# Kernel tuning notes

Hardware: AMD Instinct MI355X
Metric: run time of the kernel (lower is better)

## Reference

```python
import jax, jax.numpy as jnp
import numpy as np

NUM_BINS = 30
MIN_BW = 0.001
MIN_BH = 0.001
MIN_D = 0.001
LI, UI = 0.0, 1.0   # input bounds
LO, UO = 0.0, 1.0   # output bounds
DERIV_OUT = (UO - LO) / (UI - LI)
EPS = 1e-6


def _cumparams(unnorm, lower, upper, min_size):
    # softmax -> min-size floor -> cumsum -> pad zero -> affine to [lower, upper]
    p = jax.nn.softmax(unnorm, axis=-1)
    p = min_size + (1.0 - min_size * NUM_BINS) * p
    cp = jnp.cumsum(p, axis=-1)
    cp = jnp.pad(cp, [(0, 0), (1, 0)])            # [V, nb+1], starts at 0
    cp = (upper - lower) * cp + lower
    return cp, cp[..., 1:] - cp[..., :-1]         # cum, bin sizes


def _spline_forward(inputs, uw, uh, ud):
    V = uw.shape[0]
    cw, widths = _cumparams(uw, LI, UI, MIN_BW)   # [V, nb+1], [V, nb]
    ch, heights = _cumparams(uh, LO, UO, MIN_BH)

    # boundary derivative constant: softplus(c) = 1 - MIN_D  =>  deriv = 1 at edges
    c = np.log(np.exp(1.0 - MIN_D) - 1.0).astype(np.float32)
    edge = jnp.full((V, 1), c, dtype=uw.dtype)
    derivs = MIN_D + jax.nn.softplus(jnp.concatenate([edge, ud, edge], axis=-1))  # [V, nb+1]

    delta = heights / widths                      # [V, nb]
    cb = cw.at[..., -1].add(EPS)                  # bin-search boundaries

    below = inputs < LI
    above = inputs > UI
    inside = ~(below | above)
    x = jnp.clip(inputs, LI, UI)                  # safe values for masked-out points

    # per-point bin search: [B, V, nb+1] comparison then sum
    bin_idx = jnp.sum(x[..., None] >= cb[None], axis=-1) - 1
    bin_idx = jnp.clip(bin_idx, 0, NUM_BINS - 1)  # [B, V] int

    v = jnp.arange(V)[None, :]
    icw = cw[v, bin_idx]
    ibw = widths[v, bin_idx]
    ich = ch[v, bin_idx]
    idl = delta[v, bin_idx]
    d0 = derivs[v, bin_idx]
    d1 = derivs[v, bin_idx + 1]
    ih = heights[v, bin_idx]

    theta = (x - icw) / ibw
    t1mt = theta * (1.0 - theta)
    den = idl + (d0 + d1 - 2.0 * idl) * t1mt
    out_in = ich + ih * (idl * theta * theta + d0 * t1mt) / den
    numd = (idl * idl) * (d1 * theta * theta + 2.0 * idl * t1mt + d0 * (1.0 - theta) ** 2)
    lad_in = jnp.log(numd) - 2.0 * jnp.log(den)

    out = jnp.where(below, LO + (inputs - LI) * DERIV_OUT,
          jnp.where(above, UO + (inputs - UI) * DERIV_OUT, out_in))
    lad = jnp.where(inside, lad_in, 0.0)
    return out, lad


def setup_inputs() -> dict:
    key = jax.random.key(0)
    k1, k2, k3, k4 = jax.random.split(key, 4)
    B, V = 16384, 512
    inputs = jax.random.uniform(k1, (B, V), dtype=jnp.float32)
    uw = 0.3 * jax.random.normal(k2, (V, NUM_BINS), dtype=jnp.float32)
    uh = 0.3 * jax.random.normal(k3, (V, NUM_BINS), dtype=jnp.float32)
    ud = 0.5405 + 0.1 * jax.random.normal(k4, (V, NUM_BINS - 1), dtype=jnp.float32)
    return {"inputs": inputs, "unnormalized_widths": uw,
            "unnormalized_heights": uh, "unnormalized_derivatives": ud}


def reference(inputs, unnormalized_widths, unnormalized_heights, unnormalized_derivatives):
    return _spline_forward(inputs, unnormalized_widths, unnormalized_heights,
                           unnormalized_derivatives)
```

## Files before the change

### kernel.cpp

```cpp
#include <hip/hip_runtime.h>
#include <math.h>

#define NB 30
#define PS 99
#define TPB 256

typedef float f32x4 __attribute__((ext_vector_type(4)));

__device__ float g_par[512 * PS];

__device__ __forceinline__ float softplus_f(float x) {
    return fmaxf(x, 0.0f) + log1pf(__expf(-fabsf(x)));
}

__device__ __forceinline__ void stage_cum(const float* __restrict__ u, int v,
                                          float* __restrict__ dst) {
    float e[NB];
#pragma unroll
    for (int k = 0; k < NB; ++k) e[k] = u[v * NB + k];
    float m = e[0];
#pragma unroll
    for (int k = 1; k < NB; ++k) m = fmaxf(m, e[k]);
    float s = 0.f;
#pragma unroll
    for (int k = 0; k < NB; ++k) { e[k] = __expf(e[k] - m); s += e[k]; }
    const float fac = (1.0f - 0.001f * (float)NB) / s;
    float run = 0.f;
    dst[0] = 0.f;
#pragma unroll
    for (int k = 0; k < NB; ++k) {
        run += 0.001f + fac * e[k];
        dst[3 * (k + 1)] = run;
    }
}

__device__ __forceinline__ void col_params(const float* __restrict__ uw,
                                           const float* __restrict__ uh,
                                           const float* __restrict__ ud,
                                           int v, float* __restrict__ pcw) {
    stage_cum(uw, v, pcw);
    stage_cum(uh, v, pcw + 1);
    pcw[2] = 1.0f;
    pcw[3 * NB + 2] = 1.0f;
#pragma unroll
    for (int k = 1; k < NB; ++k)
        pcw[3 * k + 2] = 0.001f + softplus_f(ud[v * (NB - 1) + k - 1]);
    pcw[93] = 3.0e38f;
    pcw[94] = 0.f; pcw[95] = 0.f; pcw[96] = 0.f; pcw[97] = 0.f; pcw[98] = 0.f;
}

__global__ void rqs_params_kernel(const float* __restrict__ uw,
                                  const float* __restrict__ uh,
                                  const float* __restrict__ ud, int V) {
    const int v = blockIdx.x * 64 + threadIdx.x;
    if (v < V) col_params(uw, uh, ud, v, &g_par[v * PS]);
}

__device__ __forceinline__ void spline_eval(float cwl, float chl, float d0,
                                            float cwr, float chr, float d1,
                                            float xq, float xraw,
                                            float& o, float& ldv) {
    const float wd = cwr - cwl;
    const float h  = chr - chl;
    const float winv = __builtin_amdgcn_rcpf(wd);
    const float delta = h * winv;
    const float theta = (xq - cwl) * winv;
    const float omt = 1.0f - theta;
    const float t1mt = theta * omt;
    const float th2 = theta * theta;
    const float den = delta + (d0 + d1 - 2.0f * delta) * t1mt;
    const float dinv = __builtin_amdgcn_rcpf(den);
    const float oi = chl + h * (delta * th2 + d0 * t1mt) * dinv;
    const float numd = delta * delta * (d1 * th2 + 2.0f * delta * t1mt + d0 * omt * omt);
    const float li = __logf(numd * dinv * dinv);
    const bool inside = (xraw >= 0.0f) && (xraw <= 1.0f);
    o   = inside ? oi : xraw;
    ldv = inside ? li : 0.0f;
}

__global__ __launch_bounds__(TPB, 8) void rqs_main_kernel(
        const float* __restrict__ x_in, float* __restrict__ out,
        float* __restrict__ lad, int B) {
    const int V = 512;
    __shared__ f32x4 pkS4[32 * PS / 4];
    float* pkS = (float*)pkS4;

    const int tid = threadIdx.x;
    const int colTile = blockIdx.x & 15;
    const int rowBlk  = blockIdx.x >> 4;

    const f32x4* __restrict__ gp4 = (const f32x4*)&g_par[colTile * 32 * PS];
    for (int i = tid; i < 792; i += TPB) pkS4[i] = gp4[i];
    __syncthreads();

    const int c = tid & 31;
    const int rsub = tid >> 5;
    const int col = colTile * 32 + c;
    const float* __restrict__ pc = &pkS[c * PS];

    const float c12 = pc[12], c24 = pc[24], c36 = pc[36], c48 = pc[48];
    const float c60 = pc[60], c72 = pc[72], c84 = pc[84];

    for (int r0 = rowBlk * 32 + rsub * 4; r0 < B; r0 += 4096) {
        float xv[4], xq[4];
        int jj[4];
#pragma unroll
        for (int u = 0; u < 4; ++u) {
            const int row = r0 + u;
            xv[u] = (row < B) ? x_in[(size_t)row * V + col] : 0.5f;
        }
#pragma unroll
        for (int u = 0; u < 4; ++u) xq[u] = fminf(fmaxf(xv[u], 0.0f), 1.0f);

#pragma unroll
        for (int u = 0; u < 4; ++u) {
            const float xx = xq[u];
            const bool b1 = (c48 <= xx);
            const float l2 = b1 ? c72 : c24;
            const bool b2 = (l2 <= xx);
            const float l3 = b1 ? (b2 ? c84 : c60) : (b2 ? c36 : c12);
            const bool b3 = (l3 <= xx);
            jj[u] = (b1 ? 48 : 0) + (b2 ? 24 : 0) + (b3 ? 12 : 0);
        }
#pragma unroll
        for (int u = 0; u < 4; ++u) jj[u] += (pc[jj[u] + 6] <= xq[u]) ? 6 : 0;
#pragma unroll
        for (int u = 0; u < 4; ++u) jj[u] += (pc[jj[u] + 3] <= xq[u]) ? 3 : 0;
#pragma unroll
        for (int u = 0; u < 4; ++u) jj[u] = min(jj[u], 87);

        float cwl[4], chl[4], d0a[4], cwr[4], chr[4], d1a[4];
#pragma unroll
        for (int u = 0; u < 4; ++u) {
            const float* p = pc + jj[u];
            cwl[u] = p[0]; chl[u] = p[1]; d0a[u] = p[2];
            cwr[u] = p[3]; chr[u] = p[4]; d1a[u] = p[5];
        }

#pragma unroll
        for (int u = 0; u < 4; ++u) {
            const int row = r0 + u;
            if (row >= B) continue;
            float o, ldv;
            spline_eval(cwl[u], chl[u], d0a[u], cwr[u], chr[u], d1a[u],
                        xq[u], xv[u], o, ldv);
            out[(size_t)row * V + col] = o;
            lad[(size_t)row * V + col] = ldv;
        }
    }
}

__global__ __launch_bounds__(TPB, 4) void rqs_gen_kernel(
        const float* __restrict__ x_in, const float* __restrict__ uw,
        const float* __restrict__ uh, const float* __restrict__ ud,
        float* __restrict__ out, float* __restrict__ lad,
        int B, int V, int nct, int rowTiles) {
    __shared__ float pkS[64 * PS];

    const int tid = threadIdx.x;
    const int colTile = blockIdx.x % nct;
    const int rowBlk  = blockIdx.x / nct;
    const int colbase = colTile * 64;

    if (tid < 64 && colbase + tid < V)
        col_params(uw, uh, ud, colbase + tid, &pkS[tid * PS]);
    __syncthreads();

    const int c = tid & 63;
    const int w = tid >> 6;
    const int col = colbase + c;
    if (col >= V) return;
    const float* __restrict__ pc = &pkS[c * PS];

    for (int row = rowBlk * 4 + w; row < B; row += rowTiles * 4) {
        const float xr = x_in[(size_t)row * V + col];
        const float xq = fminf(fmaxf(xr, 0.0f), 1.0f);
        int j = (pc[48] <= xq) ? 48 : 0;
        j += (pc[j + 24] <= xq) ? 24 : 0;
        j += (pc[j + 12] <= xq) ? 12 : 0;
        j += (pc[j +  6] <= xq) ?  6 : 0;
        j += (pc[j +  3] <= xq) ?  3 : 0;
        j = min(j, 87);
        const float* p = pc + j;
        float o, ldv;
        spline_eval(p[0], p[1], p[2], p[3], p[4], p[5], xq, xr, o, ldv);
        out[(size_t)row * V + col] = o;
        lad[(size_t)row * V + col] = ldv;
    }
}

extern "C" void kernel_launch(void* const* d_in, const int* in_sizes, int n_in,
                              void* d_out, int out_size, void* d_ws, size_t ws_size,
                              hipStream_t stream) {
    const float* x  = (const float*)d_in[0];
    const float* uw = (const float*)d_in[1];
    const float* uh = (const float*)d_in[2];
    const float* ud = (const float*)d_in[3];

    const int V = in_sizes[1] / NB;
    const int B = in_sizes[0] / V;

    float* out = (float*)d_out;
    float* lad = out + (size_t)B * V;

    if (V == 512) {
        rqs_params_kernel<<<8, 64, 0, stream>>>(uw, uh, ud, V);
        rqs_main_kernel<<<2048, TPB, 0, stream>>>(x, out, lad, B);
    } else {
        const int nct = (V + 63) / 64;
        int rowTiles = (B + 3) / 4;
        if (rowTiles > 128) rowTiles = 128;
        rqs_gen_kernel<<<nct * rowTiles, TPB, 0, stream>>>(
            x, uw, uh, ud, out, lad, B, V, nct, rowTiles);
    }
}
```

Before: 36.25 us.

## Precompute per-bin spline coefficients as packed float4 records and retile main kernel

The params kernel now computes, for each bin, the left knot, reciprocal width, left height, bin height, delta, the denominator coefficient and both derivatives. It stores them as two float4 records per bin, plus a sentinel. The main kernel runs a 5-level binary search over bin starts and fetches the two records with vector LDS loads. This removes per-element width/height subtraction, one reciprocal and several multiplies, and drops the clamp step. Each block now covers 16 columns by 64 rows instead of 32 columns, which halves the contiguous span per row segment in global accesses. The fast path is now limited to B divisible by 64.

```diff
diff --git a/kernel.cpp b/kernel.cpp
--- a/kernel.cpp
+++ b/kernel.cpp
@@ -2,19 +2,20 @@
 #include <math.h>
 
 #define NB 30
+#define RQ 67
 #define PS 99
 #define TPB 256
 
 typedef float f32x4 __attribute__((ext_vector_type(4)));
 
-__device__ float g_par[512 * PS];
+__device__ f32x4 g_rec[512 * RQ];
 
 __device__ __forceinline__ float softplus_f(float x) {
     return fmaxf(x, 0.0f) + log1pf(__expf(-fabsf(x)));
 }
 
-__device__ __forceinline__ void stage_cum(const float* __restrict__ u, int v,
-                                          float* __restrict__ dst) {
+__device__ __forceinline__ void cum_col(const float* __restrict__ u, int v,
+                                        float* __restrict__ dst ) {
     float e[NB];
 #pragma unroll
     for (int k = 0; k < NB; ++k) e[k] = u[v * NB + k];
@@ -30,36 +31,126 @@
 #pragma unroll
     for (int k = 0; k < NB; ++k) {
         run += 0.001f + fac * e[k];
-        dst[3 * (k + 1)] = run;
-    }
-}
-
-__device__ __forceinline__ void col_params(const float* __restrict__ uw,
-                                           const float* __restrict__ uh,
-                                           const float* __restrict__ ud,
-                                           int v, float* __restrict__ pcw) {
-    stage_cum(uw, v, pcw);
-    stage_cum(uh, v, pcw + 1);
-    pcw[2] = 1.0f;
-    pcw[3 * NB + 2] = 1.0f;
-#pragma unroll
-    for (int k = 1; k < NB; ++k)
-        pcw[3 * k + 2] = 0.001f + softplus_f(ud[v * (NB - 1) + k - 1]);
-    pcw[93] = 3.0e38f;
-    pcw[94] = 0.f; pcw[95] = 0.f; pcw[96] = 0.f; pcw[97] = 0.f; pcw[98] = 0.f;
+        dst[k + 1] = run;
+    }
 }
 
 __global__ void rqs_params_kernel(const float* __restrict__ uw,
                                   const float* __restrict__ uh,
                                   const float* __restrict__ ud, int V) {
     const int v = blockIdx.x * 64 + threadIdx.x;
-    if (v < V) col_params(uw, uh, ud, v, &g_par[v * PS]);
-}
-
-__device__ __forceinline__ void spline_eval(float cwl, float chl, float d0,
-                                            float cwr, float chr, float d1,
-                                            float xq, float xraw,
-                                            float& o, float& ldv) {
+    if (v >= V) return;
+    float cw[NB + 1], ch[NB + 1], dv[NB + 1];
+    cum_col(uw, v, cw);
+    cum_col(uh, v, ch);
+    dv[0] = 1.0f;
+    dv[NB] = 1.0f;
+#pragma unroll
+    for (int k = 1; k < NB; ++k)
+        dv[k] = 0.001f + softplus_f(ud[v * (NB - 1) + k - 1]);
+
+    f32x4* dst = &g_rec[v * RQ];
+#pragma unroll
+    for (int j = 0; j < NB; ++j) {
+        const float w = cw[j + 1] - cw[j];
+        const float h = ch[j + 1] - ch[j];
+        const float winv = 1.0f / w;
+        const float delta = h * winv;
+        f32x4 A, Bq;
+        A.x = cw[j]; A.y = winv; A.z = ch[j]; A.w = h;
+        Bq.x = delta; Bq.y = dv[j] + dv[j + 1] - 2.0f * delta;
+        Bq.z = dv[j]; Bq.w = dv[j + 1];
+        dst[2 * j] = A;
+        dst[2 * j + 1] = Bq;
+    }
+    f32x4 sent; sent.x = 3.0e38f; sent.y = 0.f; sent.z = 0.f; sent.w = 0.f;
+    dst[2 * NB] = sent;
+}
+
+__global__ __launch_bounds__(TPB, 8) void rqs_main_kernel(
+        const float* __restrict__ x_in, float* __restrict__ out,
+        float* __restrict__ lad, int B, int rowBlks) {
+    const int V = 512;
+    __shared__ f32x4 pkS[16 * RQ];
+
+    const int tid = threadIdx.x;
+    const int colTile = blockIdx.x & 31;
+    const int rowBlk  = blockIdx.x >> 5;
+
+    const f32x4* __restrict__ gp = &g_rec[(size_t)colTile * 16 * RQ];
+    for (int i = tid; i < 16 * RQ; i += TPB) pkS[i] = gp[i];
+    __syncthreads();
+
+    const int c = tid & 15;
+    const int rsub = tid >> 4;
+    const int col = colTile * 16 + c;
+    const f32x4* __restrict__ qv = &pkS[c * RQ];
+    const float* __restrict__ qf = (const float*)qv;
+
+    const float h4 = qf[4 * 8],  h8 = qf[8 * 8],  h12 = qf[12 * 8];
+    const float h16 = qf[16 * 8], h20 = qf[20 * 8], h24 = qf[24 * 8], h28 = qf[28 * 8];
+
+    for (int row0 = rowBlk * 64 + rsub * 4; row0 < B; row0 += rowBlks * 64) {
+        float xv[4];
+        int jj[4];
+#pragma unroll
+        for (int u = 0; u < 4; ++u) xv[u] = x_in[(size_t)(row0 + u) * V + col];
+
+#pragma unroll
+        for (int u = 0; u < 4; ++u) {
+            const float xx = xv[u];
+            const bool b1 = (h16 <= xx);
+            const float l2 = b1 ? h24 : h8;
+            const bool b2 = (l2 <= xx);
+            const float l3 = b1 ? (b2 ? h28 : h20) : (b2 ? h12 : h4);
+            const bool b3 = (l3 <= xx);
+            jj[u] = (b1 ? 16 : 0) + (b2 ? 8 : 0) + (b3 ? 4 : 0);
+        }
+#pragma unroll
+        for (int u = 0; u < 4; ++u) jj[u] += (qf[(jj[u] + 2) * 8] <= xv[u]) ? 2 : 0;
+#pragma unroll
+        for (int u = 0; u < 4; ++u) jj[u] += (qf[(jj[u] + 1) * 8] <= xv[u]) ? 1 : 0;
+
+#pragma unroll
+        for (int g = 0; g < 2; ++g) {
+            f32x4 A[2], Bq[2];
+#pragma unroll
+            for (int q = 0; q < 2; ++q) {
+                const int idx = 2 * jj[g * 2 + q];
+                A[q]  = qv[idx];
+                Bq[q] = qv[idx + 1];
+            }
+#pragma unroll
+            for (int q = 0; q < 2; ++q) {
+                const int u = g * 2 + q;
+                const float x = xv[u];
+                const float theta = (x - A[q].x) * A[q].y;
+                const float omt  = 1.0f - theta;
+                const float th2  = theta * theta;
+                const float t1mt = theta * omt;
+                const float den  = __builtin_fmaf(Bq[q].y, t1mt, Bq[q].x);
+                const float dinv = __builtin_amdgcn_rcpf(den);
+                float tmp = __builtin_fmaf(Bq[q].z, t1mt, Bq[q].x * th2);
+                const float oi = __builtin_fmaf(A[q].w, tmp * dinv, A[q].z);
+                const float c2 = Bq[q].x * t1mt;
+                float nb = __builtin_fmaf(Bq[q].w, th2, c2 + c2);
+                nb = __builtin_fmaf(Bq[q].z, omt * omt, nb);
+                const float numd = (Bq[q].x * Bq[q].x) * nb;
+                const float li = __logf(numd * (dinv * dinv));
+
+                const bool inside = (x >= 0.0f) && (x <= 1.0f);
+                const size_t o_idx = (size_t)(row0 + u) * V + col;
+                out[o_idx] = inside ? oi : x;
+                lad[o_idx] = inside ? li : 0.0f;
+            }
+        }
+    }
+}
+
+__device__ __forceinline__ void spline_eval_g(const float* p, float xq, float xraw,
+                                              float& o, float& ldv) {
+    const float cwl = p[0], chl = p[1], d0 = p[2];
+    const float cwr = p[3], chr = p[4], d1 = p[5];
     const float wd = cwr - cwl;
     const float h  = chr - chl;
     const float winv = __builtin_amdgcn_rcpf(wd);
@@ -78,78 +169,6 @@
     ldv = inside ? li : 0.0f;
 }
 
-__global__ __launch_bounds__(TPB, 8) void rqs_main_kernel(
-        const float* __restrict__ x_in, float* __restrict__ out,
-        float* __restrict__ lad, int B) {
-    const int V = 512;
-    __shared__ f32x4 pkS4[32 * PS / 4];
-    float* pkS = (float*)pkS4;
-
-    const int tid = threadIdx.x;
-    const int colTile = blockIdx.x & 15;
-    const int rowBlk  = blockIdx.x >> 4;
-
-    const f32x4* __restrict__ gp4 = (const f32x4*)&g_par[colTile * 32 * PS];
-    for (int i = tid; i < 792; i += TPB) pkS4[i] = gp4[i];
-    __syncthreads();
-
-    const int c = tid & 31;
-    const int rsub = tid >> 5;
-    const int col = colTile * 32 + c;
-    const float* __restrict__ pc = &pkS[c * PS];
-
-    const float c12 = pc[12], c24 = pc[24], c36 = pc[36], c48 = pc[48];
-    const float c60 = pc[60], c72 = pc[72], c84 = pc[84];
-
-    for (int r0 = rowBlk * 32 + rsub * 4; r0 < B; r0 += 4096) {
-        float xv[4], xq[4];
-        int jj[4];
-#pragma unroll
-        for (int u = 0; u < 4; ++u) {
-            const int row = r0 + u;
-            xv[u] = (row < B) ? x_in[(size_t)row * V + col] : 0.5f;
-        }
-#pragma unroll
-        for (int u = 0; u < 4; ++u) xq[u] = fminf(fmaxf(xv[u], 0.0f), 1.0f);
-
-#pragma unroll
-        for (int u = 0; u < 4; ++u) {
-            const float xx = xq[u];
-            const bool b1 = (c48 <= xx);
-            const float l2 = b1 ? c72 : c24;
-            const bool b2 = (l2 <= xx);
-            const float l3 = b1 ? (b2 ? c84 : c60) : (b2 ? c36 : c12);
-            const bool b3 = (l3 <= xx);
-            jj[u] = (b1 ? 48 : 0) + (b2 ? 24 : 0) + (b3 ? 12 : 0);
-        }
-#pragma unroll
-        for (int u = 0; u < 4; ++u) jj[u] += (pc[jj[u] + 6] <= xq[u]) ? 6 : 0;
-#pragma unroll
-        for (int u = 0; u < 4; ++u) jj[u] += (pc[jj[u] + 3] <= xq[u]) ? 3 : 0;
-#pragma unroll
-        for (int u = 0; u < 4; ++u) jj[u] = min(jj[u], 87);
-
-        float cwl[4], chl[4], d0a[4], cwr[4], chr[4], d1a[4];
-#pragma unroll
-        for (int u = 0; u < 4; ++u) {
-            const float* p = pc + jj[u];
-            cwl[u] = p[0]; chl[u] = p[1]; d0a[u] = p[2];
-            cwr[u] = p[3]; chr[u] = p[4]; d1a[u] = p[5];
-        }
-
-#pragma unroll
-        for (int u = 0; u < 4; ++u) {
-            const int row = r0 + u;
-            if (row >= B) continue;
-            float o, ldv;
-            spline_eval(cwl[u], chl[u], d0a[u], cwr[u], chr[u], d1a[u],
-                        xq[u], xv[u], o, ldv);
-            out[(size_t)row * V + col] = o;
-            lad[(size_t)row * V + col] = ldv;
-        }
-    }
-}
-
 __global__ __launch_bounds__(TPB, 4) void rqs_gen_kernel(
         const float* __restrict__ x_in, const float* __restrict__ uw,
         const float* __restrict__ uh, const float* __restrict__ ud,
@@ -162,8 +181,21 @@
     const int rowBlk  = blockIdx.x / nct;
     const int colbase = colTile * 64;
 
-    if (tid < 64 && colbase + tid < V)
-        col_params(uw, uh, ud, colbase + tid, &pkS[tid * PS]);
+    if (tid < 64 && colbase + tid < V) {
+        const int v = colbase + tid;
+        float cw[NB + 1], ch[NB + 1];
+        cum_col(uw, v, cw);
+        cum_col(uh, v, ch);
+        float* pcw = &pkS[tid * PS];
+#pragma unroll
+        for (int k = 0; k <= NB; ++k) { pcw[3 * k] = cw[k]; pcw[3 * k + 1] = ch[k]; }
+        pcw[2] = 1.0f;
+        pcw[3 * NB + 2] = 1.0f;
+#pragma unroll
+        for (int k = 1; k < NB; ++k)
+            pcw[3 * k + 2] = 0.001f + softplus_f(ud[v * (NB - 1) + k - 1]);
+        pcw[93] = 3.0e38f;
+    }
     __syncthreads();
 
     const int c = tid & 63;
@@ -181,9 +213,8 @@
         j += (pc[j +  6] <= xq) ?  6 : 0;
         j += (pc[j +  3] <= xq) ?  3 : 0;
         j = min(j, 87);
-        const float* p = pc + j;
         float o, ldv;
-        spline_eval(p[0], p[1], p[2], p[3], p[4], p[5], xq, xr, o, ldv);
+        spline_eval_g(pc + j, xq, xr, o, ldv);
         out[(size_t)row * V + col] = o;
         lad[(size_t)row * V + col] = ldv;
     }
@@ -203,9 +234,11 @@
     float* out = (float*)d_out;
     float* lad = out + (size_t)B * V;
 
-    if (V == 512) {
+    if (V == 512 && (B % 64) == 0 && B >= 64) {
         rqs_params_kernel<<<8, 64, 0, stream>>>(uw, uh, ud, V);
-        rqs_main_kernel<<<2048, TPB, 0, stream>>>(x, out, lad, B);
+        int rowBlks = B / 64;
+        if (rowBlks > 64) rowBlks = 64;
+        rqs_main_kernel<<<32 * rowBlks, TPB, 0, stream>>>(x, out, lad, B, rowBlks);
     } else {
         const int nct = (V + 63) / 64;
         int rowTiles = (B + 3) / 4;
```

Result: slower. 41.92 us (+15.6%).
